# Optimization experiments

Measured on AMD Instinct MI355X. Metric: run time of the kernel, lower is better.

Reference implementation:

```python
import jax, jax.numpy as jnp
import numpy as np

NPOINT = 2048
K = 16
EPS = 1e-5


def farthest_point_sample(xyz, npoint):
    # xyz: (B, N, 3) -> (B, npoint) int32 indices. Deterministic start at index 0.
    B, N, _ = xyz.shape
    batch = jnp.arange(B)

    def step(carry, _):
        dists, far = carry                      # (B,N), (B,)
        centroid = xyz[batch, far]              # (B,3)
        d = jnp.sum((xyz - centroid[:, None, :]) ** 2, axis=-1)  # (B,N)
        dists = jnp.minimum(dists, d)
        nxt = jnp.argmax(dists, axis=-1).astype(jnp.int32)
        return (dists, nxt), far

    init = (jnp.full((B, N), 1e10, xyz.dtype), jnp.zeros((B,), jnp.int32))
    _, idx = jax.lax.scan(step, init, None, length=npoint)
    return jnp.transpose(idx)                   # (B, npoint)


def knn_query(k, xyz, query_xyz):
    # squared-distance KNN via matmul form (same ordering as torch.cdist+topk smallest)
    x2 = jnp.sum(xyz * xyz, axis=-1)            # (B,N)
    q2 = jnp.sum(query_xyz * query_xyz, axis=-1)  # (B,S)
    sqd = q2[:, :, None] + x2[:, None, :] - 2.0 * jnp.einsum('bsd,bnd->bsn', query_xyz, xyz)
    _, idx = jax.lax.top_k(-sqd, k)             # smallest k distances
    return idx                                  # (B,S,k)


def layer_norm(x, g, b):
    mu = jnp.mean(x, axis=-1, keepdims=True)
    var = jnp.mean((x - mu) ** 2, axis=-1, keepdims=True)
    return (x - mu) * jax.lax.rsqrt(var + EPS) * g + b


def setup_inputs() -> dict:
    key = jax.random.key(0)
    ks = jax.random.split(key, 6)
    B, N, IN_DIM, OUT_DIM = 4, 8192, 64, 128
    C_IN = 3 + IN_DIM
    s1 = 1.0 / np.sqrt(C_IN)
    s2 = 1.0 / np.sqrt(OUT_DIM)
    return {
        'xyz': jax.random.normal(ks[0], (B, N, 3), jnp.float32),
        'feat': jax.random.normal(ks[1], (B, N, IN_DIM), jnp.float32),
        'W1': jax.random.uniform(ks[2], (C_IN, OUT_DIM), jnp.float32, -s1, s1),
        'b1': jax.random.uniform(ks[3], (OUT_DIM,), jnp.float32, -s1, s1),
        'W2': jax.random.uniform(ks[4], (OUT_DIM, OUT_DIM), jnp.float32, -s2, s2),
        'b2': jax.random.uniform(ks[5], (OUT_DIM,), jnp.float32, -s2, s2),
        'ln_g': jnp.ones((OUT_DIM,), jnp.float32),
        'ln_b': jnp.zeros((OUT_DIM,), jnp.float32),
    }


def reference(xyz, feat, W1, b1, W2, b2, ln_g, ln_b):
    B = xyz.shape[0]
    bidx = jnp.arange(B)[:, None, None]

    fps_idx = farthest_point_sample(xyz, NPOINT)                 # (B,S)
    new_xyz = jnp.take_along_axis(xyz, fps_idx[:, :, None], axis=1)  # (B,S,3)
    knn_idx = knn_query(K, xyz, new_xyz)                         # (B,S,K)

    grp_xyz = xyz[bidx, knn_idx] - new_xyz[:, :, None, :]        # (B,S,K,3)
    grp_feat = feat[bidx, knn_idx]                               # (B,S,K,in_dim)
    grouped = jnp.concatenate([grp_xyz, grp_feat], axis=-1)      # (B,S,K,3+in_dim)

    h = jax.nn.relu(grouped @ W1 + b1)
    h = h @ W2 + b2                                              # (B,S,K,out_dim)
    new_feat = jnp.max(h, axis=2)                                # (B,S,out_dim)
    return new_xyz, layer_norm(new_feat, ln_g, ln_b)
```

## Files before the change

### kernel.cpp

```cpp
#include <hip/hip_runtime.h>
#include <stdint.h>

#define BB 4
#define NN 8192
#define SS 2048
#define KK 16
#define IND 64
#define CIN 67
#define OD 128

typedef unsigned int   u32;
typedef unsigned long long u64;
typedef float f2 __attribute__((ext_vector_type(2)));

__global__ __launch_bounds__(256) void k_prep(const float* __restrict__ xyz,
                                              float4* __restrict__ pts){
  int i = blockIdx.x * 256 + threadIdx.x;
  if (i >= BB*NN) return;
  float x = xyz[3*i+0];
  float y = xyz[3*i+1];
  float z = xyz[3*i+2];
  float x2 = __fadd_rn(__fadd_rn(__fmul_rn(x,x), __fmul_rn(y,y)), __fmul_rn(z,z));
  pts[i] = make_float4(x,y,z,x2);
}

template<int CTRL>
__device__ __forceinline__ float dpp_mv(float x){
  int xi = __builtin_bit_cast(int, x);
  int r  = __builtin_amdgcn_update_dpp(xi, xi, CTRL, 0xf, 0xf, false);
  return __builtin_bit_cast(float, r);
}

#define FPT 512
#define PPT (NN/FPT)
#define NW  (FPT/64)
__global__ __launch_bounds__(FPT) void k_fps(const float4* __restrict__ pts,
                                             float* __restrict__ out_xyz,
                                             float* __restrict__ fps_xyz){
  #pragma clang fp contract(off)
  extern __shared__ float smem[];
  float* sx = smem;
  float* sy = smem +   NN;
  float* sz = smem + 2*NN;
  __shared__ u64 pkey[2][NW];
  int b = blockIdx.x;
  int tid = threadIdx.x;
  int wid = tid >> 6, lane = tid & 63;
  const float4* P = pts + (size_t)b*NN;
  f2 X[PPT/2], Y[PPT/2], Z[PPT/2], D[PPT/2];
  #pragma unroll
  for (int jp=0;jp<PPT/2;jp++){
    int n0 = tid*PPT + 2*jp;
    float4 p0 = P[n0];
    float4 p1 = P[n0+1];
    X[jp] = (f2){p0.x, p1.x};
    Y[jp] = (f2){p0.y, p1.y};
    Z[jp] = (f2){p0.z, p1.z};
    D[jp] = (f2){1e10f, 1e10f};
    sx[n0]=p0.x; sx[n0+1]=p1.x;
    sy[n0]=p0.y; sy[n0+1]=p1.y;
    sz[n0]=p0.z; sz[n0+1]=p1.z;
  }
  float4 p0v = P[0];
  float cx=p0v.x, cy=p0v.y, cz=p0v.z;
  size_t ob = (size_t)b*SS*3;
  if (tid==0){
    out_xyz[ob+0]=cx; out_xyz[ob+1]=cy; out_xyz[ob+2]=cz;
    fps_xyz[ob+0]=cx; fps_xyz[ob+1]=cy; fps_xyz[ob+2]=cz;
  }
  __syncthreads();

  for (int it=1; it<SS; ++it){
    f2 mm = (f2){-1.0f, -1.0f};
    #pragma unroll
    for (int jp=0;jp<PPT/2;jp++){
      f2 dx = X[jp] - cx;
      f2 dy = Y[jp] - cy;
      f2 dz = Z[jp] - cz;
      f2 d  = ((dx*dx) + (dy*dy)) + (dz*dz);
      f2 nd = __builtin_elementwise_min(D[jp], d);
      D[jp] = nd;
      mm = __builtin_elementwise_max(mm, nd);
    }
    float md = fmaxf(mm.x, mm.y);
    float m = md;
    m = fmaxf(m, dpp_mv<0x111>(m));
    m = fmaxf(m, dpp_mv<0x112>(m));
    m = fmaxf(m, dpp_mv<0x114>(m));
    m = fmaxf(m, dpp_mv<0x118>(m));
    m = fmaxf(m, dpp_mv<0x142>(m));
    m = fmaxf(m, dpp_mv<0x143>(m));
    float wmax = __builtin_bit_cast(float,
        __builtin_amdgcn_readlane(__builtin_bit_cast(int, m), 63));
    u64 ball = __ballot(md == wmax);
    int wl = __ffsll((unsigned long long)ball) - 1;
    int bj = 0;
    if (md == wmax){
      #pragma unroll
      for (int t=PPT-1;t>=0;--t){
        float v = (t&1)? D[t>>1].y : D[t>>1].x;
        if (v == wmax) bj = t;
      }
    }
    int widx = __shfl(tid*PPT + bj, wl, 64);
    if (lane==0){
      pkey[it&1][wid] = ((u64)__float_as_uint(wmax) << 32) | (u32)~(u32)widx;
    }
    __syncthreads();
    u64 bk = pkey[it&1][0];
    #pragma unroll
    for (int w=1;w<NW;w++){
      u64 k2 = pkey[it&1][w];
      if (k2 > bk) bk = k2;
    }
    int gw = (int)~(u32)bk;
    cx = sx[gw]; cy = sy[gw]; cz = sz[gw];
    if (tid==0){
      size_t o = ob + (size_t)it*3;
      out_xyz[o]=cx; out_xyz[o+1]=cy; out_xyz[o+2]=cz;
      fps_xyz[o]=cx; fps_xyz[o+1]=cy; fps_xyz[o+2]=cz;
    }
  }
}

__global__ __launch_bounds__(256) void k_knn(const float4* __restrict__ pts,
                                             const float* __restrict__ fps_xyz,
                                             int* __restrict__ knn_idx){
  int q = blockIdx.x*4 + (threadIdx.x>>6);
  int lane = threadIdx.x & 63;
  int b = q / SS;
  const float4* P = pts + (size_t)b*NN;
  float qx=fps_xyz[3*q], qy=fps_xyz[3*q+1], qz=fps_xyz[3*q+2];
  float q2 = __fadd_rn(__fadd_rn(__fmul_rn(qx,qx),__fmul_rn(qy,qy)),__fmul_rn(qz,qz));
  u64 key[KK];
  #pragma unroll
  for (int t=0;t<KK;t++) key[t] = ~0ull;
  for (int i=0;i<NN/64;i++){
    int n = i*64 + lane;
    float4 p = P[n];
    float dot = __fadd_rn(__fadd_rn(__fmul_rn(qx,p.x),__fmul_rn(qy,p.y)),__fmul_rn(qz,p.z));
    float sd  = __fsub_rn(__fadd_rn(q2,p.w), __fmul_rn(2.0f,dot));
    u32 bu = __float_as_uint(sd);
    bu ^= (u32)((int)bu >> 31) | 0x80000000u;
    u64 kk = ((u64)bu<<32) | (u32)n;
    if (kk < key[KK-1]){
      key[KK-1] = kk;
      #pragma unroll
      for (int t=KK-1;t>0;--t){
        u64 a=key[t-1], c=key[t];
        bool sw = c < a;
        key[t-1] = sw? c : a;
        key[t]   = sw? a : c;
      }
    }
  }
  #pragma unroll 1
  for (int r=0;r<KK;r++){
    u64 m = key[0];
    #pragma unroll
    for (int mm=1;mm<64;mm<<=1){
      u64 om = __shfl_xor((unsigned long long)m, mm, 64);
      if (om < m) m = om;
    }
    if (lane==0) knn_idx[q*KK + r] = (int)(u32)m;
    if (key[0]==m){
      #pragma unroll
      for (int t=0;t<KK-1;t++) key[t]=key[t+1];
      key[KK-1]=~0ull;
    }
  }
}

__global__ __launch_bounds__(256) void k_mlp(const float* __restrict__ feat,
                                             const float4* __restrict__ pts,
                                             const float* __restrict__ fps_xyz,
                                             const int* __restrict__ knn_idx,
                                             const float* __restrict__ W1, const float* __restrict__ b1,
                                             const float* __restrict__ W2, const float* __restrict__ b2,
                                             const float* __restrict__ g_ln, const float* __restrict__ b_ln,
                                             float* __restrict__ out_feat){
  __shared__ float gbuf[4][CIN][16];
  __shared__ float hbuf[4][OD][20];
  int wid = threadIdx.x>>6, lane = threadIdx.x&63;
  int q = blockIdx.x*4 + wid;
  int b = q / SS;
  float* gw = &gbuf[wid][0][0];
  float* hw = &hbuf[wid][0][0];
  int k = lane & 15, part = lane >> 4;
  int n = knn_idx[q*KK + k];
  {
    const float* fp = feat + ((size_t)b*NN + (size_t)n)*IND + part*16;
    float4 f0 = *(const float4*)(fp+0);
    float4 f1 = *(const float4*)(fp+4);
    float4 f2v = *(const float4*)(fp+8);
    float4 f3 = *(const float4*)(fp+12);
    float v[16] = {f0.x,f0.y,f0.z,f0.w, f1.x,f1.y,f1.z,f1.w,
                   f2v.x,f2v.y,f2v.z,f2v.w, f3.x,f3.y,f3.z,f3.w};
    #pragma unroll
    for (int c=0;c<16;c++) gw[(3+part*16+c)*16 + k] = v[c];
    if (part==0){
      float4 p = pts[(size_t)b*NN + n];
      gw[0*16+k] = __fsub_rn(p.x, fps_xyz[3*q+0]);
      gw[1*16+k] = __fsub_rn(p.y, fps_xyz[3*q+1]);
      gw[2*16+k] = __fsub_rn(p.z, fps_xyz[3*q+2]);
    }
  }
  __syncthreads();
  int o = lane;
  float a0[16], a1[16];
  #pragma unroll
  for (int t=0;t<16;t++){ a0[t]=0.0f; a1[t]=0.0f; }
  #pragma unroll 4
  for (int j=0;j<CIN;j++){
    float w0 = W1[j*OD + o];
    float w1 = W1[j*OD + o + 64];
    #pragma unroll
    for (int t=0;t<16;t++){
      float gv = gw[j*16+t];
      a0[t]=fmaf(gv,w0,a0[t]); a1[t]=fmaf(gv,w1,a1[t]);
    }
  }
  float bb0 = b1[o], bb1 = b1[o+64];
  #pragma unroll
  for (int t=0;t<16;t++){
    hw[o*20+t]      = fmaxf(a0[t]+bb0, 0.0f);
    hw[(o+64)*20+t] = fmaxf(a1[t]+bb1, 0.0f);
  }
  __syncthreads();
  float c0[16], c1[16];
  #pragma unroll
  for (int t=0;t<16;t++){ c0[t]=0.0f; c1[t]=0.0f; }
  #pragma unroll 4
  for (int j=0;j<OD;j++){
    float w0 = W2[j*OD + o];
    float w1 = W2[j*OD + o + 64];
    #pragma unroll
    for (int t=0;t<16;t++){
      float hv = hw[j*20+t];
      c0[t]=fmaf(hv,w0,c0[t]); c1[t]=fmaf(hv,w1,c1[t]);
    }
  }
  float m0=c0[0], m1=c1[0];
  #pragma unroll
  for (int t=1;t<16;t++){ m0=fmaxf(m0,c0[t]); m1=fmaxf(m1,c1[t]); }
  m0 += b2[o]; m1 += b2[o+64];
  float ssum = m0+m1;
  #pragma unroll
  for (int mm=1;mm<64;mm<<=1) ssum += __shfl_xor(ssum,mm,64);
  float mean = ssum * (1.0f/128.0f);
  float d0=m0-mean, d1=m1-mean;
  float sq = d0*d0 + d1*d1;
  #pragma unroll
  for (int mm=1;mm<64;mm<<=1) sq += __shfl_xor(sq,mm,64);
  float var = sq * (1.0f/128.0f);
  float x = var + 1e-5f;
  float r = rsqrtf(x);
  r = r * (1.5f - 0.5f*x*r*r);
  size_t obf = (size_t)q*OD;
  out_feat[obf+o]    = fmaf(d0*r, g_ln[o],    b_ln[o]);
  out_feat[obf+o+64] = fmaf(d1*r, g_ln[o+64], b_ln[o+64]);
}

extern "C" void kernel_launch(void* const* d_in, const int* in_sizes, int n_in,
                              void* d_out, int out_size, void* d_ws, size_t ws_size,
                              hipStream_t stream){
  const float* xyz  = (const float*)d_in[0];
  const float* feat = (const float*)d_in[1];
  const float* W1   = (const float*)d_in[2];
  const float* b1   = (const float*)d_in[3];
  const float* W2   = (const float*)d_in[4];
  const float* b2   = (const float*)d_in[5];
  const float* lg   = (const float*)d_in[6];
  const float* lb   = (const float*)d_in[7];
  float* out = (float*)d_out;
  char* ws = (char*)d_ws;
  float4* pts = (float4*)ws;
  float*  fpsx = (float*)(ws + 524288);
  int*    kidx = (int*)(ws + 524288 + 98304);
  float* out_xyz  = out;
  float* out_feat = out + (size_t)BB*SS*3;

  hipFuncSetAttribute((const void*)k_fps,
                      hipFuncAttributeMaxDynamicSharedMemorySize, 3*NN*4);

  hipLaunchKernelGGL(k_prep, dim3((BB*NN+255)/256), dim3(256), 0, stream, xyz, pts);
  hipLaunchKernelGGL(k_fps,  dim3(BB),              dim3(FPT), 3*NN*4, stream, pts, out_xyz, fpsx);
  hipLaunchKernelGGL(k_knn,  dim3(BB*SS/4),         dim3(256), 0, stream, pts, fpsx, kidx);
  hipLaunchKernelGGL(k_mlp,  dim3(BB*SS/4),         dim3(256), 0, stream,
                     feat, pts, fpsx, kidx, W1, b1, W2, b2, lg, lb, out_feat);
}
```

Before: 2.440 ms.

## Fuse KNN into MLP kernel and buffer FPS centroids in LDS

The KNN and MLP kernels are merged, so each wave's selected neighbour indices stay in registers and are used directly for the gather. This removes the knn_idx global round trip and one launch. FPS now stores its centroids in LDS and writes them out in one coalesced pass at the end, instead of a serial tid==0 global store every iteration. The fused kernel keeps the gather/MLP shared buffers live during the KNN phase, which may lower occupancy.

After: 2.498 ms. +2.4%, slower.

```diff
diff --git a/kernel.cpp b/kernel.cpp
--- a/kernel.cpp
+++ b/kernel.cpp
@@ -34,14 +34,17 @@
 #define FPT 512
 #define PPT (NN/FPT)
 #define NW  (FPT/64)
+#define FPS_LDS ((3*NN + 3*SS)*4)
 __global__ __launch_bounds__(FPT) void k_fps(const float4* __restrict__ pts,
-                                             float* __restrict__ out_xyz,
-                                             float* __restrict__ fps_xyz){
+                                             float* __restrict__ out_xyz){
   #pragma clang fp contract(off)
   extern __shared__ float smem[];
   float* sx = smem;
   float* sy = smem +   NN;
   float* sz = smem + 2*NN;
+  float* rx = smem + 3*NN;
+  float* ry = smem + 3*NN +   SS;
+  float* rz = smem + 3*NN + 2*SS;
   __shared__ u64 pkey[2][NW];
   int b = blockIdx.x;
   int tid = threadIdx.x;
@@ -63,11 +66,7 @@
   }
   float4 p0v = P[0];
   float cx=p0v.x, cy=p0v.y, cz=p0v.z;
-  size_t ob = (size_t)b*SS*3;
-  if (tid==0){
-    out_xyz[ob+0]=cx; out_xyz[ob+1]=cy; out_xyz[ob+2]=cz;
-    fps_xyz[ob+0]=cx; fps_xyz[ob+1]=cy; fps_xyz[ob+2]=cz;
-  }
+  if (tid==0){ rx[0]=cx; ry[0]=cy; rz[0]=cz; }
   __syncthreads();
 
   for (int it=1; it<SS; ++it){
@@ -115,22 +114,29 @@
     }
     int gw = (int)~(u32)bk;
     cx = sx[gw]; cy = sy[gw]; cz = sz[gw];
-    if (tid==0){
-      size_t o = ob + (size_t)it*3;
-      out_xyz[o]=cx; out_xyz[o+1]=cy; out_xyz[o+2]=cz;
-      fps_xyz[o]=cx; fps_xyz[o+1]=cy; fps_xyz[o+2]=cz;
-    }
-  }
-}
-
-__global__ __launch_bounds__(256) void k_knn(const float4* __restrict__ pts,
-                                             const float* __restrict__ fps_xyz,
-                                             int* __restrict__ knn_idx){
-  int q = blockIdx.x*4 + (threadIdx.x>>6);
-  int lane = threadIdx.x & 63;
+    if (tid==0){ rx[it]=cx; ry[it]=cy; rz[it]=cz; }
+  }
+  __syncthreads();
+  for (int i=tid; i<SS; i+=FPT){
+    size_t o = (size_t)b*SS*3 + (size_t)i*3;
+    out_xyz[o]=rx[i]; out_xyz[o+1]=ry[i]; out_xyz[o+2]=rz[i];
+  }
+}
+
+__global__ __launch_bounds__(256) void k_knn_mlp(const float4* __restrict__ pts,
+                                                 const float* __restrict__ ctr,
+                                                 const float* __restrict__ feat,
+                                                 const float* __restrict__ W1, const float* __restrict__ b1,
+                                                 const float* __restrict__ W2, const float* __restrict__ b2,
+                                                 const float* __restrict__ g_ln, const float* __restrict__ b_ln,
+                                                 float* __restrict__ out_feat){
+  __shared__ float gbuf[4][CIN][16];
+  __shared__ float hbuf[4][OD][20];
+  int wid = threadIdx.x>>6, lane = threadIdx.x&63;
+  int q = blockIdx.x*4 + wid;
   int b = q / SS;
   const float4* P = pts + (size_t)b*NN;
-  float qx=fps_xyz[3*q], qy=fps_xyz[3*q+1], qz=fps_xyz[3*q+2];
+  float qx=ctr[3*q], qy=ctr[3*q+1], qz=ctr[3*q+2];
   float q2 = __fadd_rn(__fadd_rn(__fmul_rn(qx,qx),__fmul_rn(qy,qy)),__fmul_rn(qz,qz));
   u64 key[KK];
   #pragma unroll
@@ -154,6 +160,8 @@
       }
     }
   }
+  int k = lane & 15, part = lane >> 4;
+  int n_sel = 0;
   #pragma unroll 1
   for (int r=0;r<KK;r++){
     u64 m = key[0];
@@ -162,34 +170,17 @@
       u64 om = __shfl_xor((unsigned long long)m, mm, 64);
       if (om < m) m = om;
     }
-    if (lane==0) knn_idx[q*KK + r] = (int)(u32)m;
+    if (k == r) n_sel = (int)(u32)m;
     if (key[0]==m){
       #pragma unroll
       for (int t=0;t<KK-1;t++) key[t]=key[t+1];
       key[KK-1]=~0ull;
     }
   }
-}
-
-__global__ __launch_bounds__(256) void k_mlp(const float* __restrict__ feat,
-                                             const float4* __restrict__ pts,
-                                             const float* __restrict__ fps_xyz,
-                                             const int* __restrict__ knn_idx,
-                                             const float* __restrict__ W1, const float* __restrict__ b1,
-                                             const float* __restrict__ W2, const float* __restrict__ b2,
-                                             const float* __restrict__ g_ln, const float* __restrict__ b_ln,
-                                             float* __restrict__ out_feat){
-  __shared__ float gbuf[4][CIN][16];
-  __shared__ float hbuf[4][OD][20];
-  int wid = threadIdx.x>>6, lane = threadIdx.x&63;
-  int q = blockIdx.x*4 + wid;
-  int b = q / SS;
   float* gw = &gbuf[wid][0][0];
   float* hw = &hbuf[wid][0][0];
-  int k = lane & 15, part = lane >> 4;
-  int n = knn_idx[q*KK + k];
   {
-    const float* fp = feat + ((size_t)b*NN + (size_t)n)*IND + part*16;
+    const float* fp = feat + ((size_t)b*NN + (size_t)n_sel)*IND + part*16;
     float4 f0 = *(const float4*)(fp+0);
     float4 f1 = *(const float4*)(fp+4);
     float4 f2v = *(const float4*)(fp+8);
@@ -199,10 +190,10 @@
     #pragma unroll
     for (int c=0;c<16;c++) gw[(3+part*16+c)*16 + k] = v[c];
     if (part==0){
-      float4 p = pts[(size_t)b*NN + n];
-      gw[0*16+k] = __fsub_rn(p.x, fps_xyz[3*q+0]);
-      gw[1*16+k] = __fsub_rn(p.y, fps_xyz[3*q+1]);
-      gw[2*16+k] = __fsub_rn(p.z, fps_xyz[3*q+2]);
+      float4 p = P[n_sel];
+      gw[0*16+k] = __fsub_rn(p.x, qx);
+      gw[1*16+k] = __fsub_rn(p.y, qy);
+      gw[2*16+k] = __fsub_rn(p.z, qz);
     }
   }
   __syncthreads();
@@ -273,19 +264,15 @@
   const float* lg   = (const float*)d_in[6];
   const float* lb   = (const float*)d_in[7];
   float* out = (float*)d_out;
-  char* ws = (char*)d_ws;
-  float4* pts = (float4*)ws;
-  float*  fpsx = (float*)(ws + 524288);
-  int*    kidx = (int*)(ws + 524288 + 98304);
+  float4* pts = (float4*)d_ws;
   float* out_xyz  = out;
   float* out_feat = out + (size_t)BB*SS*3;
 
   hipFuncSetAttribute((const void*)k_fps,
-                      hipFuncAttributeMaxDynamicSharedMemorySize, 3*NN*4);
-
-  hipLaunchKernelGGL(k_prep, dim3((BB*NN+255)/256), dim3(256), 0, stream, xyz, pts);
-  hipLaunchKernelGGL(k_fps,  dim3(BB),              dim3(FPT), 3*NN*4, stream, pts, out_xyz, fpsx);
-  hipLaunchKernelGGL(k_knn,  dim3(BB*SS/4),         dim3(256), 0, stream, pts, fpsx, kidx);
-  hipLaunchKernelGGL(k_mlp,  dim3(BB*SS/4),         dim3(256), 0, stream,
-                     feat, pts, fpsx, kidx, W1, b1, W2, b2, lg, lb, out_feat);
-}
+                      hipFuncAttributeMaxDynamicSharedMemorySize, FPS_LDS);
+
+  hipLaunchKernelGGL(k_prep,    dim3((BB*NN+255)/256), dim3(256), 0,       stream, xyz, pts);
+  hipLaunchKernelGGL(k_fps,     dim3(BB),              dim3(FPT), FPS_LDS, stream, pts, out_xyz);
+  hipLaunchKernelGGL(k_knn_mlp, dim3(BB*SS/4),         dim3(256), 0,       stream,
+                     pts, out_xyz, feat, W1, b1, W2, b2, lg, lb, out_feat);
+}
```
